# Optimization experiments

Measured on AMD Instinct MI355X. Metric: run time of the kernel, lower is better.

Reference implementation:

```python
import jax, jax.numpy as jnp
import numpy as np

D_MODEL = 2048
NUM_HEADS = 16
HEAD_DIM = D_MODEL // NUM_HEADS
SCALE = HEAD_DIM ** -0.5
ALPHA = 1.0


def setup_inputs() -> dict:
    key = jax.random.key(0)
    ks = jax.random.split(key, 9)
    B, T = 2, 2048
    s = 0.02
    w = lambda k: jax.random.normal(k, (D_MODEL, D_MODEL), jnp.float32) * s
    b = lambda k: jax.random.normal(k, (D_MODEL,), jnp.float32) * s
    return {
        'x': jax.random.normal(ks[0], (B, T, D_MODEL), jnp.float32),
        'q_w': w(ks[1]), 'q_b': b(ks[2]),
        'k_w': w(ks[3]), 'k_b': b(ks[4]),
        'v_w': w(ks[5]), 'v_b': b(ks[6]),
        'o_w': w(ks[7]), 'o_b': b(ks[8]),
    }


def reference(x, q_w, q_b, k_w, k_b, v_w, v_b, o_w, o_b):
    B, T, D = x.shape
    H, HD = NUM_HEADS, HEAD_DIM

    def proj_split(w, bias):
        y = x @ w.T + bias  # torch Linear: x @ W^T + b
        # B T (H D) -> (B H) T D
        return y.reshape(B, T, H, HD).transpose(0, 2, 1, 3).reshape(B * H, T, HD)

    Q = proj_split(q_w, q_b)
    K = proj_split(k_w, k_b)
    V = proj_split(v_w, v_b)

    # Note: original computes S[h,i,j] = K_i . Q_j (K first, Q second)
    S = jnp.einsum('hid,hjd->hij', K, Q) * SCALE  # (B*H, T, T)

    idx = jnp.arange(T)
    delta = idx[:, None] - idx[None, :]  # delta[i,j] = i - j
    # similarity_power_law decay: -(delta**alpha) for delta>=0, else 0
    decay = jnp.where(delta < 0, 0.0, -(delta.astype(jnp.float32) ** ALPHA))
    # causal mask: positions with j > i (delta < 0) set to -inf, then add decay
    S = jnp.where(delta < 0, -jnp.inf, S) + decay

    C = jax.nn.softmax(S, axis=-1)
    attn = jnp.einsum('hij,hjd->hid', C, V)  # (B*H, T, HD)
    # (B H) T D -> B T (H D)
    attn = attn.reshape(B, H, T, HD).transpose(0, 2, 1, 3).reshape(B, T, D)
    return attn @ o_w.T + o_b
```

## Files before the change

### kernel.cpp

```cpp
#include <hip/hip_runtime.h>
#include <hip/hip_bf16.h>
#include <stdint.h>

#define BT    4096
#define DM    2048
#define TSEQ  2048
#define NHEAD 16
#define HD    128
#define QKV_LD 6144
#define ATT_SCALE 0.088388347648318447f
#define WIN   64

typedef __attribute__((ext_vector_type(8))) short short8;
typedef __attribute__((ext_vector_type(4))) float f32x4;

__device__ __forceinline__ uint16_t f2bf(float f) {
  uint32_t u = __float_as_uint(f);
  return (uint16_t)((u + 0x7FFFu + ((u >> 16) & 1u)) >> 16);
}

__device__ __forceinline__ void gload_lds16(const void* g, void* l) {
  __builtin_amdgcn_global_load_lds((__attribute__((address_space(1))) void*)g,
                                   (__attribute__((address_space(3))) void*)l,
                                   16, 0, 0);
}

__global__ __launch_bounds__(256) void prep(const float* __restrict__ x,
                                            const float* __restrict__ qw,
                                            const float* __restrict__ kw,
                                            const float* __restrict__ vw,
                                            const float* __restrict__ ow,
                                            const float* __restrict__ qb,
                                            const float* __restrict__ kb,
                                            const float* __restrict__ vb,
                                            uint16_t* __restrict__ xb,
                                            uint16_t* __restrict__ wqkv,
                                            uint16_t* __restrict__ wo,
                                            float* __restrict__ bcat) {
  const int NX = BT * DM / 4;
  const int NW = DM * DM / 4;
  const int total = NX + 4 * NW;
  int i0 = blockIdx.x * 256 + threadIdx.x;
  for (int idx = i0; idx < total; idx += gridDim.x * 256) {
    const float* src;
    uint16_t* dst;
    int off;
    if (idx < NX)            { src = x;  dst = xb;                          off = idx; }
    else if (idx < NX + NW)  { src = qw; dst = wqkv;                        off = idx - NX; }
    else if (idx < NX + 2*NW){ src = kw; dst = wqkv + (size_t)DM * DM;      off = idx - NX - NW; }
    else if (idx < NX + 3*NW){ src = vw; dst = wqkv + (size_t)2 * DM * DM;  off = idx - NX - 2*NW; }
    else                     { src = ow; dst = wo;                          off = idx - NX - 3*NW; }
    float4 v = ((const float4*)src)[off];
    ushort4 o;
    o.x = f2bf(v.x); o.y = f2bf(v.y); o.z = f2bf(v.z); o.w = f2bf(v.w);
    ((ushort4*)dst)[off] = o;
  }
  if (i0 < 3 * DM) {
    float v = (i0 < DM) ? qb[i0] : (i0 < 2 * DM ? kb[i0 - DM] : vb[i0 - 2 * DM]);
    bcat[i0] = v;
  }
}

template <int MB_, bool OUT_BF16>
__global__ __launch_bounds__(256, 2) void gemm128(const uint16_t* __restrict__ A,
                                                  const uint16_t* __restrict__ B,
                                                  const float* __restrict__ bias,
                                                  void* __restrict__ Cout,
                                                  int M, int N, int K) {
  __shared__ uint16_t sm[4 * 8192];

  const int tid = threadIdx.x;
  const int l   = tid & 63;
  const int wid = tid >> 6;
  const int wr  = wid >> 1;
  const int wc  = wid & 1;
  const int ln  = l & 15;
  const int g   = l >> 4;

  constexpr int NB_ = 8 / MB_;
  const int nbx    = N >> 7;
  const int nbm    = M >> 7;
  const int bid    = blockIdx.x;
  const int xcd    = bid & 7;
  const int idx    = bid >> 3;
  const int rect_n = nbx / NB_;
  const int rect_m = nbm / MB_;
  const int m_t    = (xcd / NB_) * rect_m + idx / rect_n;
  const int n_t    = (xcd % NB_) * rect_n + idx % rect_n;
  const int m0     = m_t << 7;
  const int n0     = n_t << 7;

  const int srow = l >> 2;
  const int gch  = (l & 3) ^ ((l >> 3) & 3);
  const uint16_t* pa0 = A + (size_t)(m0 + wid * 16 + srow) * K + gch * 8;
  const uint16_t* pa1 = pa0 + (size_t)64 * K;
  const uint16_t* pb0 = B + (size_t)(n0 + wid * 16 + srow) * K + gch * 8;
  const uint16_t* pb1 = pb0 + (size_t)64 * K;
  const int la0 = wid * 512;
  const int la1 = 2048 + wid * 512;
  const int lb0 = 4096 + wid * 512;
  const int lb1 = 6144 + wid * 512;

  const int pc = g ^ ((ln >> 1) & 3);

  f32x4 acc[4][4];
#pragma unroll
  for (int i = 0; i < 4; ++i)
#pragma unroll
    for (int j = 0; j < 4; ++j) acc[i][j] = (f32x4){0.f, 0.f, 0.f, 0.f};

  const int nt = K >> 5;

#define STAGE(T)                                                        \
  {                                                                     \
    uint16_t* base_ = sm + (size_t)((T) & 3) * 8192;                    \
    const size_t ko_ = (size_t)(T) * 32;                                \
    gload_lds16(pa0 + ko_, base_ + la0);                                \
    gload_lds16(pa1 + ko_, base_ + la1);                                \
    gload_lds16(pb0 + ko_, base_ + lb0);                                \
    gload_lds16(pb1 + ko_, base_ + lb1);                                \
  }

#define COMPUTE(T)                                                      \
  {                                                                     \
    const uint16_t* buf_ = sm + (size_t)((T) & 3) * 8192;               \
    short8 af_[4], bf_[4];                                              \
    _Pragma("unroll")                                                   \
    for (int fi = 0; fi < 4; ++fi)                                      \
      af_[fi] = *(const short8*)(buf_ + (wr * 64 + fi * 16 + ln) * 32 + pc * 8); \
    _Pragma("unroll")                                                   \
    for (int fj = 0; fj < 4; ++fj)                                      \
      bf_[fj] = *(const short8*)(buf_ + 4096 + (wc * 64 + fj * 16 + ln) * 32 + pc * 8); \
    __builtin_amdgcn_s_setprio(1);                                      \
    _Pragma("unroll")                                                   \
    for (int fi = 0; fi < 4; ++fi)                                      \
      _Pragma("unroll")                                                 \
      for (int fj = 0; fj < 4; ++fj)                                    \
        acc[fi][fj] = __builtin_amdgcn_mfma_f32_16x16x32_bf16(          \
            af_[fi], bf_[fj], acc[fi][fj], 0, 0, 0);                    \
    __builtin_amdgcn_s_setprio(0);                                      \
  }

  STAGE(0); STAGE(1); STAGE(2);
  asm volatile("s_waitcnt vmcnt(8)" ::: "memory");
  __builtin_amdgcn_s_barrier();

#pragma unroll 1
  for (int t = 0; t < nt - 3; ++t) {
    STAGE(t + 3);
    COMPUTE(t);
    asm volatile("s_waitcnt vmcnt(8)" ::: "memory");
    __builtin_amdgcn_s_barrier();
  }
  COMPUTE(nt - 3);
  asm volatile("s_waitcnt vmcnt(4)" ::: "memory");
  __builtin_amdgcn_s_barrier();
  COMPUTE(nt - 2);
  asm volatile("s_waitcnt vmcnt(0)" ::: "memory");
  __builtin_amdgcn_s_barrier();
  COMPUTE(nt - 1);
#undef STAGE
#undef COMPUTE

  const int g4 = g * 4;
#pragma unroll
  for (int fi = 0; fi < 4; ++fi) {
    size_t row = (size_t)(m0 + wr * 64 + fi * 16 + g4);
#pragma unroll
    for (int fj = 0; fj < 4; ++fj) {
      int col = n0 + wc * 64 + fj * 16 + ln;
      float bv = bias[col];
#pragma unroll
      for (int r = 0; r < 4; ++r) {
        float v = acc[fi][fj][r] + bv;
        if (OUT_BF16) ((uint16_t*)Cout)[(row + r) * N + col] = f2bf(v);
        else          ((float*)Cout)[(row + r) * N + col] = v;
      }
    }
  }
}

__global__ __launch_bounds__(256) void attn_mfma(const uint16_t* __restrict__ QKV,
                                                 uint16_t* __restrict__ O) {
  __shared__ __align__(16) uint16_t smem[16384 + 17408];
  uint16_t* Qs = smem;
  uint16_t* Vt = smem + 16384;
  uint16_t* Pl = smem;

  const int tid  = threadIdx.x;
  const int lane = tid & 63;
  const int w    = tid >> 6;
  const int g    = lane >> 4;
  const int ln   = lane & 15;

  const int i0 = blockIdx.x * 64;
  const int h  = blockIdx.y;
  const int b  = blockIdx.z;
  const int wb = i0 - 63;
  const size_t hoff  = (size_t)h * HD;
  const size_t bbase = (size_t)b * TSEQ;

#pragma unroll
  for (int it = 0; it < 8; ++it) {
    int s   = it * 256 + tid;
    int row = s >> 4, c = s & 15;
    int j = wb + row;
    if (j >= 0 && j < TSEQ) {
      const uint16_t* gsrc = QKV + (bbase + j) * (size_t)QKV_LD + hoff
                           + (size_t)((c ^ (row & 7)) * 8);
      uint16_t* ldst = Qs + (size_t)(s & ~63) * 8;
      gload_lds16(gsrc, ldst);
    } else {
      uint4 z = {0, 0, 0, 0};
      *(uint4*)(Qs + (size_t)s * 8) = z;
    }
  }

#pragma unroll
  for (int it = 0; it < 4; ++it) {
    int s  = it * 256 + tid;
    int jp = (s & 15) | (it << 4);
    int dc = (s >> 4) & 15;
    int j0 = wb + 2 * jp;
    uint4 va = {0, 0, 0, 0}, vb = {0, 0, 0, 0};
    if (j0 >= 0 && j0 < TSEQ)
      va = *(const uint4*)(QKV + (bbase + j0) * (size_t)QKV_LD + 2 * DM + hoff + dc * 8);
    if (j0 + 1 >= 0 && j0 + 1 < TSEQ)
      vb = *(const uint4*)(QKV + (bbase + j0 + 1) * (size_t)QKV_LD + 2 * DM + hoff + dc * 8);
    const uint16_t* ap = (const uint16_t*)&va;
    const uint16_t* bp = (const uint16_t*)&vb;
#pragma unroll
    for (int t = 0; t < 8; ++t) {
      uint32_t pk = (uint32_t)ap[t] | ((uint32_t)bp[t] << 16);
      *(uint32_t*)(Vt + (size_t)(dc * 8 + t) * 136 + 2 * jp) = pk;
    }
  }

  short8 kreg[4];
  {
    const uint16_t* kp = QKV + (bbase + i0 + w * 16 + ln) * (size_t)QKV_LD
                       + DM + hoff + g * 8;
#pragma unroll
    for (int kc = 0; kc < 4; ++kc) kreg[kc] = *(const short8*)(kp + kc * 32);
  }

  __syncthreads();

  f32x4 acc[8];
#pragma unroll
  for (int nf = 0; nf < 8; ++nf) acc[nf] = (f32x4){0.f, 0.f, 0.f, 0.f};
#pragma unroll
  for (int kc = 0; kc < 4; ++kc) {
#pragma unroll
    for (int nf = 0; nf < 8; ++nf) {
      int row = nf * 16 + ln;
      int chunk = (kc * 4 + g) ^ (row & 7);
      short8 qf = *(const short8*)(Qs + (size_t)row * 128 + chunk * 8);
      acc[nf] = __builtin_amdgcn_mfma_f32_16x16x32_bf16(kreg[kc], qf, acc[nf], 0, 0, 0);
    }
  }

#pragma unroll
  for (int nf = 0; nf < 8; ++nf) {
    int rj = nf * 16 + ln;
    int jg = wb + rj;
#pragma unroll
    for (int r = 0; r < 4; ++r) {
      int il = w * 16 + g * 4 + r;
      int delta = il + 63 - rj;
      float v = acc[nf][r] * ATT_SCALE - (float)delta;
      acc[nf][r] = ((unsigned)delta < 64u && jg >= 0) ? v : -1e30f;
    }
  }

  float inv[4];
#pragma unroll
  for (int r = 0; r < 4; ++r) {
    float mx = acc[0][r];
#pragma unroll
    for (int nf = 1; nf < 8; ++nf) mx = fmaxf(mx, acc[nf][r]);
    mx = fmaxf(mx, __shfl_xor(mx, 1));
    mx = fmaxf(mx, __shfl_xor(mx, 2));
    mx = fmaxf(mx, __shfl_xor(mx, 4));
    mx = fmaxf(mx, __shfl_xor(mx, 8));
    float s = 0.f;
#pragma unroll
    for (int nf = 0; nf < 8; ++nf) {
      float e = __expf(acc[nf][r] - mx);
      acc[nf][r] = e;
      s += e;
    }
    s += __shfl_xor(s, 1);
    s += __shfl_xor(s, 2);
    s += __shfl_xor(s, 4);
    s += __shfl_xor(s, 8);
    inv[r] = 1.0f / s;
  }

  __syncthreads();

#pragma unroll
  for (int nf = 0; nf < 8; ++nf)
#pragma unroll
    for (int r = 0; r < 4; ++r)
      Pl[(size_t)(w * 16 + g * 4 + r) * 136 + nf * 16 + ln] = f2bf(acc[nf][r]);
  asm volatile("s_waitcnt lgkmcnt(0)" ::: "memory");
  __builtin_amdgcn_sched_barrier(0);

  f32x4 o[8];
#pragma unroll
  for (int nf = 0; nf < 8; ++nf) o[nf] = (f32x4){0.f, 0.f, 0.f, 0.f};
#pragma unroll
  for (int kc = 0; kc < 4; ++kc) {
    short8 pa = *(const short8*)(Pl + (size_t)(w * 16 + ln) * 136 + kc * 32 + g * 8);
#pragma unroll
    for (int nf = 0; nf < 8; ++nf) {
      short8 vbf = *(const short8*)(Vt + (size_t)(nf * 16 + ln) * 136 + kc * 32 + g * 8);
      o[nf] = __builtin_amdgcn_mfma_f32_16x16x32_bf16(pa, vbf, o[nf], 0, 0, 0);
    }
  }

  const size_t obase = (bbase + i0 + w * 16) * (size_t)DM + hoff;
#pragma unroll
  for (int nf = 0; nf < 8; ++nf)
#pragma unroll
    for (int r = 0; r < 4; ++r)
      O[obase + (size_t)(g * 4 + r) * DM + nf * 16 + ln] = f2bf(o[nf][r] * inv[r]);
}

extern "C" void kernel_launch(void* const* d_in, const int* in_sizes, int n_in,
                              void* d_out, int out_size, void* d_ws, size_t ws_size,
                              hipStream_t stream) {
  const float* x   = (const float*)d_in[0];
  const float* q_w = (const float*)d_in[1];
  const float* q_b = (const float*)d_in[2];
  const float* k_w = (const float*)d_in[3];
  const float* k_b = (const float*)d_in[4];
  const float* v_w = (const float*)d_in[5];
  const float* v_b = (const float*)d_in[6];
  const float* o_w = (const float*)d_in[7];
  const float* o_b = (const float*)d_in[8];

  char* ws = (char*)d_ws;
  const size_t XB_BYTES   = (size_t)BT * DM * 2;
  const size_t W_BYTES    = (size_t)DM * DM * 2;
  const size_t WQKV_BYTES = 3 * W_BYTES;

  uint16_t* xb   = (uint16_t*)(ws);
  uint16_t* wqkv = (uint16_t*)(ws + XB_BYTES);
  uint16_t* wo   = (uint16_t*)(ws + XB_BYTES + WQKV_BYTES);
  float*    bcat = (float*)   (ws + XB_BYTES + WQKV_BYTES + W_BYTES);
  uint16_t* QKVb = (uint16_t*)(ws + XB_BYTES + WQKV_BYTES + W_BYTES + 24576);

  prep<<<2048, 256, 0, stream>>>(x, q_w, k_w, v_w, o_w, q_b, k_b, v_b,
                                 xb, wqkv, wo, bcat);

  gemm128<2, true><<<(BT / 128) * (3 * DM / 128), 256, 0, stream>>>(
      xb, wqkv, bcat, QKVb, BT, 3 * DM, DM);

  dim3 ga(TSEQ / 64, NHEAD, 2);
  attn_mfma<<<ga, 256, 0, stream>>>(QKVb, xb);

  gemm128<4, false><<<(BT / 128) * (DM / 128), 256, 0, stream>>>(
      xb, wo, o_b, d_out, BT, DM, DM);
}
```

Baseline: 209.3 us.

## Use 256x256-tile 8-wave pipelined GEMM for QKV projection

New measurement: 220.0 us. 5.1% more time.

```diff
diff --git a/kernel.cpp b/kernel.cpp
--- a/kernel.cpp
+++ b/kernel.cpp
@@ -61,6 +61,121 @@
   }
 }
 
+template <bool OUT_BF16>
+__global__ __launch_bounds__(512, 1) void gemm8p(const uint16_t* __restrict__ A,
+                                                 const uint16_t* __restrict__ B,
+                                                 const float* __restrict__ bias,
+                                                 void* __restrict__ Cout,
+                                                 int M, int N, int K) {
+  __shared__ uint16_t sm[65536];
+
+  const int tid = threadIdx.x;
+  const int l   = tid & 63;
+  const int wid = tid >> 6;
+  const int wr  = wid >> 2;
+  const int wc  = wid & 3;
+  const int ln  = l & 15;
+  const int g   = l >> 4;
+
+  const int nbx    = N >> 8;
+  const int bid    = blockIdx.x;
+  const int xcd    = bid & 7;
+  const int idx    = bid >> 3;
+  const int rect_n = nbx >> 2;
+  const int rect_m = (M >> 8) >> 1;
+  const int m_t    = (xcd >> 2) * rect_m + idx / rect_n;
+  const int n_t    = (xcd & 3) * rect_n + idx % rect_n;
+  const int m0     = m_t << 8;
+  const int n0     = n_t << 8;
+
+  const int srow = l >> 2;
+  const int gch  = (l & 3) ^ ((l >> 3) & 3);
+  const uint16_t* us0 = A + (size_t)(m0 +       wid * 16 + srow) * K + gch * 8;
+  const uint16_t* us1 = A + (size_t)(m0 + 128 + wid * 16 + srow) * K + gch * 8;
+  const uint16_t* us2 = B + (size_t)(n0 +       wid * 16 + srow) * K + gch * 8;
+  const uint16_t* us3 = B + (size_t)(n0 + 128 + wid * 16 + srow) * K + gch * 8;
+  const int ldso = wid * 512;
+
+  const int pc = g ^ ((ln >> 1) & 3);
+  const int arow_base = (ln) * 32 + pc * 8;
+  const int brow_base = ((wc & 1) * 64 + ln) * 32 + pc * 8;
+
+  f32x4 acc[8][4];
+#pragma unroll
+  for (int i = 0; i < 8; ++i)
+#pragma unroll
+    for (int j = 0; j < 4; ++j) acc[i][j] = (f32x4){0.f, 0.f, 0.f, 0.f};
+
+  const int nt = K >> 5;
+
+#define STAGEU(T, U)                                                     \
+  {                                                                      \
+    const int slot_ = (4 * (T) + (U)) & 15;                              \
+    const uint16_t* s_ = (U) == 0 ? us0 : ((U) == 1 ? us1 : ((U) == 2 ? us2 : us3)); \
+    gload_lds16(s_ + (size_t)(T) * 32, sm + slot_ * 4096 + ldso);        \
+  }
+
+#define PHASE(T, MH, SU0, SU1, LASTPH)                                   \
+  {                                                                      \
+    const uint16_t* ab_ = sm + (size_t)((4 * (T) + wr) & 15) * 4096;     \
+    const uint16_t* bb_ = sm + (size_t)((4 * (T) + 2 + (wc >> 1)) & 15) * 4096; \
+    short8 af_[4], bf_[4];                                               \
+    _Pragma("unroll")                                                    \
+    for (int fi = 0; fi < 4; ++fi)                                       \
+      af_[fi] = *(const short8*)(ab_ + arow_base + ((MH) * 64 + fi * 16) * 32); \
+    _Pragma("unroll")                                                    \
+    for (int fj = 0; fj < 4; ++fj)                                       \
+      bf_[fj] = *(const short8*)(bb_ + brow_base + (fj * 16) * 32);      \
+    if ((T) + 2 < nt) { STAGEU((T) + 2, SU0); STAGEU((T) + 2, SU1); }    \
+    __builtin_amdgcn_s_barrier();                                        \
+    asm volatile("s_waitcnt lgkmcnt(0)" ::: "memory");                   \
+    __builtin_amdgcn_sched_barrier(0);                                   \
+    __builtin_amdgcn_s_setprio(1);                                       \
+    _Pragma("unroll")                                                    \
+    for (int fi = 0; fi < 4; ++fi)                                       \
+      _Pragma("unroll")                                                  \
+      for (int fj = 0; fj < 4; ++fj)                                     \
+        acc[(MH) * 4 + fi][fj] = __builtin_amdgcn_mfma_f32_16x16x32_bf16(\
+            af_[fi], bf_[fj], acc[(MH) * 4 + fi][fj], 0, 0, 0);          \
+    __builtin_amdgcn_s_setprio(0);                                       \
+    if (LASTPH) {                                                        \
+      if ((T) < nt - 2) asm volatile("s_waitcnt vmcnt(4)" ::: "memory"); \
+      else              asm volatile("s_waitcnt vmcnt(0)" ::: "memory"); \
+    }                                                                    \
+    __builtin_amdgcn_s_barrier();                                        \
+  }
+
+  STAGEU(0, 0); STAGEU(0, 1); STAGEU(0, 2); STAGEU(0, 3);
+  STAGEU(1, 0); STAGEU(1, 1); STAGEU(1, 2); STAGEU(1, 3);
+  asm volatile("s_waitcnt vmcnt(4)" ::: "memory");
+  __builtin_amdgcn_s_barrier();
+
+#pragma unroll 1
+  for (int t = 0; t < nt; ++t) {
+    PHASE(t, 0, 0, 1, 0)
+    PHASE(t, 1, 2, 3, 1)
+  }
+#undef PHASE
+#undef STAGEU
+
+  const int g4 = g * 4;
+#pragma unroll
+  for (int fi = 0; fi < 8; ++fi) {
+    size_t row = (size_t)(m0 + wr * 128 + fi * 16 + g4);
+#pragma unroll
+    for (int fj = 0; fj < 4; ++fj) {
+      int col = n0 + wc * 64 + fj * 16 + ln;
+      float bv = bias[col];
+#pragma unroll
+      for (int r = 0; r < 4; ++r) {
+        float v = acc[fi][fj][r] + bv;
+        if (OUT_BF16) ((uint16_t*)Cout)[(row + r) * N + col] = f2bf(v);
+        else          ((float*)Cout)[(row + r) * N + col] = v;
+      }
+    }
+  }
+}
+
 template <int MB_, bool OUT_BF16>
 __global__ __launch_bounds__(256, 2) void gemm128(const uint16_t* __restrict__ A,
                                                   const uint16_t* __restrict__ B,
@@ -355,7 +470,7 @@
   prep<<<2048, 256, 0, stream>>>(x, q_w, k_w, v_w, o_w, q_b, k_b, v_b,
                                  xb, wqkv, wo, bcat);
 
-  gemm128<2, true><<<(BT / 128) * (3 * DM / 128), 256, 0, stream>>>(
+  gemm8p<true><<<(BT / 256) * (3 * DM / 256), 512, 0, stream>>>(
       xb, wqkv, bcat, QKVb, BT, 3 * DM, DM);
 
   dim3 ga(TSEQ / 64, NHEAD, 2);
```
